# Optimization experiments

Measured on AMD Instinct MI355X. Metric: run time of the kernel, lower is better.

The kernel has to match this reference:

```python
import jax, jax.numpy as jnp
import numpy as np

EPS = 1e-12  # clamp before sqrt, matching torch cdist-style euclidean_dist stability


def euclidean_dist(x, y):
    # x: (N, D), y: (M, D) -> (N, M)
    x2 = jnp.sum(x * x, axis=-1, keepdims=True)          # (N, 1)
    y2 = jnp.sum(y * y, axis=-1)                          # (M,)
    d2 = x2 + y2 - 2.0 * (x @ y.T)
    return jnp.sqrt(jnp.clip(d2, EPS))


def setup_inputs() -> dict:
    key = jax.random.key(0)
    k1, k2 = jax.random.split(key)
    B, W, H, D, M = 8, 28, 28, 128, 16384
    embedding = jax.random.normal(k1, (B * W * H, D), dtype=jnp.float32)
    memory_bank = jax.random.normal(k2, (M, D), dtype=jnp.float32)
    return {"embedding": embedding, "memory_bank": memory_bank,
            "batch_size": B, "width": W, "height": H}


def reference(embedding, memory_bank, batch_size, width, height):
    num_neighbors = 9
    B = batch_size
    D = embedding.shape[-1]
    Mb = memory_bank.shape[0]

    # get_nearest_neighbors with num_neighbors=1 (topk smallest)
    dist = euclidean_dist(embedding, memory_bank)                 # (N, M) -- dominant cost
    neg_vals, locations = jax.lax.top_k(-dist, 1)                 # smallest-1
    patch_scores = (-neg_vals).reshape(B, -1)                     # (B, P)
    locations = locations.reshape(B, -1)                          # (B, P)

    # compute_anomaly_score (num_neighbors > 1 branch)
    b = jnp.arange(B)
    max_patches = jnp.argmax(patch_scores, axis=1)                # (B,)
    emb3 = embedding.reshape(B, -1, D)
    max_patches_features = emb3[b, max_patches]                   # (B, D)
    score = patch_scores[b, max_patches]                          # (B,)
    nn_index = locations[b, max_patches]                          # (B,)
    nn_sample = memory_bank[nn_index]                             # (B, D)

    k = min(num_neighbors, Mb)
    d_nn = euclidean_dist(nn_sample, memory_bank)                 # (B, M)
    _, support_samples = jax.lax.top_k(-d_nn, k)                  # (B, k) smallest-k
    support_feats = memory_bank[support_samples]                  # (B, k, D)

    # batched euclidean dist: (B,1,D) vs (B,k,D) -> (B,k)
    x = max_patches_features[:, None, :]
    d2 = (jnp.sum(x * x, -1) + jnp.sum(support_feats * support_feats, -1)
          - 2.0 * jnp.einsum('bid,bkd->bk', x, support_feats))
    distances = jnp.sqrt(jnp.clip(d2, EPS))                       # (B, k)

    weights = (1.0 - jax.nn.softmax(distances, axis=1))[:, 0]     # (B,)
    return weights * score
```

## Files before the change

### kernel.cpp

```cpp
#include <hip/hip_runtime.h>
#include <cstdint>

#define N_EMB 6272
#define DIMD  128
#define M_BANK 16384
#define BATCH 8
#define PPB   784
#define KNN   9
#define EPSF  1e-12f
#define NKB   64

typedef unsigned long long u64;
typedef _Float16 f16x8 __attribute__((ext_vector_type(8)));
typedef _Float16 f16x2 __attribute__((ext_vector_type(2)));
typedef float    f32x4 __attribute__((ext_vector_type(4)));

static __device__ __forceinline__ u64 umin64(u64 a, u64 b) { return b < a ? b : a; }
static __device__ __forceinline__ u64 umax64(u64 a, u64 b) { return b > a ? b : a; }

static __device__ __forceinline__ void gll16(const _Float16* g, _Float16* l) {
    __builtin_amdgcn_global_load_lds(
        (__attribute__((address_space(1))) void*)(const void*)g,
        (__attribute__((address_space(3))) void*)l, 16, 0, 0);
}

static __device__ __forceinline__ float dot8(f16x8 a, f16x8 b, float c) {
#if __has_builtin(__builtin_amdgcn_fdot2)
    const f16x2* pa = (const f16x2*)&a;
    const f16x2* pb = (const f16x2*)&b;
    c = __builtin_amdgcn_fdot2(pa[0], pb[0], c, false);
    c = __builtin_amdgcn_fdot2(pa[1], pb[1], c, false);
    c = __builtin_amdgcn_fdot2(pa[2], pb[2], c, false);
    c = __builtin_amdgcn_fdot2(pa[3], pb[3], c, false);
#else
    #pragma unroll
    for (int e = 0; e < 8; ++e) c += (float)a[e] * (float)b[e];
#endif
    return c;
}

__global__ __launch_bounds__(256) void convert_kernel(
        const float* __restrict__ emb, const float* __restrict__ bank,
        _Float16* __restrict__ GAh, _Float16* __restrict__ GBh,
        float* __restrict__ x2, float* __restrict__ y2,
        u64* __restrict__ packed) {
    const int gid = blockIdx.x * 256 + threadIdx.x;
    if (gid < N_EMB) packed[gid] = ~0ull;
    const int row = gid >> 4;
    const int chunk = gid & 15;
    const float* src;
    _Float16* dh;
    float* nrm;
    int R;
    if (row < M_BANK) {
        src = bank + (size_t)row * DIMD; dh = GBh; nrm = y2; R = row;
    } else {
        R = row - M_BANK;
        src = emb + (size_t)R * DIMD; dh = GAh; nrm = x2;
    }
    float4 v0 = ((const float4*)src)[chunk * 2];
    float4 v1 = ((const float4*)src)[chunk * 2 + 1];
    float f[8] = {v0.x, v0.y, v0.z, v0.w, v1.x, v1.y, v1.z, v1.w};
    f16x8 h;
    float s = 0.f;
    #pragma unroll
    for (int e = 0; e < 8; ++e) {
        h[e] = (_Float16)f[e];
        s += f[e] * f[e];
    }
    const int q = chunk >> 2, jj = chunk & 3;
    const int jj2 = jj ^ ((R >> 1) & 3);
    *(f16x8*)(dh + (size_t)R * DIMD + q * 32 + jj2 * 8) = h;
    #pragma unroll
    for (int off = 1; off < 16; off <<= 1) s += __shfl_xor(s, off, 16);
    if (chunk == 0) nrm[R] = s;
}


static __device__ __forceinline__ void stageB(
        const _Float16* __restrict__ GBh, _Float16* dst,
        int mrow0, int h, int srow, int se8) {
    #pragma unroll
    for (int j = 0; j < 2; ++j) {
        const int row = srow + j * 64;
        #pragma unroll
        for (int q = 0; q < 2; ++q)
            gll16(GBh + (size_t)(mrow0 + row) * DIMD + h * 64 + q * 32 + se8,
                  dst + q * 4096 + row * 32 + se8);
    }
}

template<int H>
static __device__ __forceinline__ void computeB(
        const _Float16* bb, const f16x8 (&a)[4][4], f32x4 (&acc)[4][4],
        int wm, int g, int r16) {
    f16x8 b[4][2];
    #pragma unroll
    for (int fj = 0; fj < 4; ++fj) {
        const int row = wm * 64 + fj * 16 + r16;
        const int sw = (g ^ ((row >> 1) & 3)) << 3;
        b[fj][0] = *(const f16x8*)&bb[row * 32 + sw];
        b[fj][1] = *(const f16x8*)&bb[4096 + row * 32 + sw];
    }
    #pragma unroll
    for (int ks = 0; ks < 2; ++ks)
        #pragma unroll
        for (int fi = 0; fi < 4; ++fi)
            #pragma unroll
            for (int fj = 0; fj < 4; ++fj)
                acc[fi][fj] = __builtin_amdgcn_mfma_f32_16x16x32_f16(
                    a[fi][2 * H + ks], b[fj][ks], acc[fi][fj], 0, 0, 0);
}

__global__ __launch_bounds__(256, 2) void dist_min_mfma(
        const _Float16* __restrict__ GAh, const _Float16* __restrict__ GBh,
        const float* __restrict__ x2, const float* __restrict__ y2,
        u64* __restrict__ packed) {
    __shared__ _Float16 smem[16384];

    const int bid = blockIdx.x;
    const int c   = bid & 15;
    const int nt  = bid >> 4;
    const int n0  = nt * 128;
    const int mbase = c * 1024;

    const int tid  = threadIdx.x;
    const int lane = tid & 63;
    const int wid  = tid >> 6;
    const int wn = wid >> 1, wm = wid & 1;
    const int g = lane >> 4, r16 = lane & 15;
    const int srow = tid >> 2;
    const int se8  = (tid & 3) * 8;

    _Float16* sB0 = smem;
    _Float16* sB1 = smem + 8192;

    float xs[4][4];
    #pragma unroll
    for (int fi = 0; fi < 4; ++fi)
        #pragma unroll
        for (int r = 0; r < 4; ++r)
            xs[fi][r] = x2[n0 + wn * 64 + fi * 16 + g * 4 + r];

    f16x8 a[4][4];
    #pragma unroll
    for (int h = 0; h < 2; ++h) {
        #pragma unroll
        for (int k = 0; k < 2; ++k)
            #pragma unroll
            for (int j = 0; j < 2; ++j) {
                const int row = srow + j * 64;
                gll16(GAh + (size_t)(n0 + row) * DIMD + (h * 2 + k) * 32 + se8,
                      smem + k * 4096 + row * 32 + se8);
            }
        __syncthreads();
        #pragma unroll
        for (int fi = 0; fi < 4; ++fi) {
            const int row = wn * 64 + fi * 16 + r16;
            const int sw = (g ^ ((row >> 1) & 3)) << 3;
            #pragma unroll
            for (int k = 0; k < 2; ++k)
                a[fi][h * 2 + k] = *(const f16x8*)&smem[k * 4096 + row * 32 + sw];
        }
        __syncthreads();
    }

    stageB(GBh, sB0, mbase, 0, srow, se8);
    __syncthreads();

    f32x4 acc[4][4];
    #pragma unroll
    for (int fi = 0; fi < 4; ++fi)
        #pragma unroll
        for (int fj = 0; fj < 4; ++fj)
            acc[fi][fj] = (f32x4){0.f, 0.f, 0.f, 0.f};

    float runmin[4][4];
    int   runidx[4][4];
    #pragma unroll
    for (int fi = 0; fi < 4; ++fi)
        #pragma unroll
        for (int r = 0; r < 4; ++r) { runmin[fi][r] = 3.4e38f; runidx[fi][r] = 0; }

    for (int t = 0; t < 8; ++t) {
        const int mt = mbase + t * 128;
        stageB(GBh, sB1, mt, 1, srow, se8);
        computeB<0>(sB0, a, acc, wm, g, r16);
        __syncthreads();
        if (t < 7) stageB(GBh, sB0, mt + 128, 0, srow, se8);
        float ys[4];
        #pragma unroll
        for (int fj = 0; fj < 4; ++fj)
            ys[fj] = y2[mt + wm * 64 + fj * 16 + r16];
        computeB<1>(sB1, a, acc, wm, g, r16);

        const int mwave = mt + wm * 64 + r16;
        #pragma unroll
        for (int fi = 0; fi < 4; ++fi) {
            #pragma unroll
            for (int r = 0; r < 4; ++r) {
                float d0 = fmaxf(fmaf(-2.f, acc[fi][0][r], xs[fi][r] + ys[0]), EPSF);
                float d1 = fmaxf(fmaf(-2.f, acc[fi][1][r], xs[fi][r] + ys[1]), EPSF);
                float d2v = fmaxf(fmaf(-2.f, acc[fi][2][r], xs[fi][r] + ys[2]), EPSF);
                float d3 = fmaxf(fmaf(-2.f, acc[fi][3][r], xs[fi][r] + ys[3]), EPSF);
                float m01 = fminf(d0, d1);  int i01 = d1 < d0 ? 1 : 0;
                float m23 = fminf(d2v, d3); int i23 = d3 < d2v ? 3 : 2;
                float tm  = fminf(m01, m23); int ti = m23 < m01 ? i23 : i01;
                if (tm < runmin[fi][r]) {
                    runmin[fi][r] = tm;
                    runidx[fi][r] = mwave + ti * 16;
                }
            }
            #pragma unroll
            for (int fj = 0; fj < 4; ++fj)
                acc[fi][fj] = (f32x4){0.f, 0.f, 0.f, 0.f};
        }
        __syncthreads();
    }

    #pragma unroll
    for (int fi = 0; fi < 4; ++fi) {
        #pragma unroll
        for (int r = 0; r < 4; ++r) {
            const int n = n0 + wn * 64 + fi * 16 + g * 4 + r;
            u64 best = ((u64)__float_as_uint(runmin[fi][r]) << 32)
                     | (unsigned)runidx[fi][r];
            #pragma unroll
            for (int off = 1; off < 16; off <<= 1)
                best = umin64(best, (u64)__shfl_xor((unsigned long long)best, off));
            if (r16 == 0) atomicMin(&packed[n], best);
        }
    }
}

__global__ __launch_bounds__(256) void knn_kernel(
        const u64* __restrict__ packed,
        const _Float16* __restrict__ GBh,
        const float* __restrict__ y2,
        u64* __restrict__ cand) {
    const int b = blockIdx.y, tid = threadIdx.x;
    __shared__ u64 red[256];
    __shared__ u64 red4[4];
    __shared__ u64 s_wkey;
    __shared__ unsigned s_nn;
    __shared__ _Float16 nv[DIMD];

    u64 bk = 0;
    for (int p = tid; p < PPB; p += 256) {
        u64 pk = packed[(size_t)b * PPB + p];
        u64 key = ((pk >> 32) << 32) | (u64)(0xFFFFFFFFu - (unsigned)p);
        bk = umax64(bk, key);
    }
    red[tid] = bk; __syncthreads();
    for (int s = 128; s; s >>= 1) {
        if (tid < s) red[tid] = umax64(red[tid], red[tid + s]);
        __syncthreads();
    }
    if (tid == 0) {
        unsigned p = 0xFFFFFFFFu - (unsigned)red[0];
        s_nn = (unsigned)packed[(size_t)b * PPB + p];
    }
    __syncthreads();
    const unsigned nn = s_nn;
    if (tid < DIMD) nv[tid] = GBh[(size_t)nn * DIMD + tid];
    __syncthreads();

    const int m = blockIdx.x * 256 + tid;
    const int delta = (((nn >> 1) ^ (m >> 1)) & 3);
    const _Float16* row = GBh + (size_t)m * DIMD;
    float dot = 0.f;
    #pragma unroll
    for (int q = 0; q < 4; ++q)
        #pragma unroll
        for (int jj2 = 0; jj2 < 4; ++jj2) {
            f16x8 ym = *(const f16x8*)(row + q * 32 + jj2 * 8);
            f16x8 xm = *(const f16x8*)&nv[q * 32 + (jj2 ^ delta) * 8];
            dot = dot8(ym, xm, dot);
        }
    float d2 = fmaxf(y2[nn] + y2[m] - 2.0f * dot, EPSF);
    const u64 mykey = ((u64)__float_as_uint(d2) << 32) | (unsigned)m;

    u64* myout = cand + ((size_t)b * NKB + blockIdx.x) * KNN;
    bool used = false;
    for (int r = 0; r < KNN; ++r) {
        u64 h = used ? ~0ull : mykey;
        #pragma unroll
        for (int off = 1; off < 64; off <<= 1)
            h = umin64(h, (u64)__shfl_xor((unsigned long long)h, off));
        if ((tid & 63) == 0) red4[tid >> 6] = h;
        __syncthreads();
        if (tid == 0) {
            u64 w = umin64(umin64(red4[0], red4[1]), umin64(red4[2], red4[3]));
            s_wkey = w;
            myout[r] = w;
        }
        __syncthreads();
        if (!used && mykey == s_wkey) used = true;
    }
}

__global__ __launch_bounds__(256) void final_kernel(
        const u64* __restrict__ packed,
        const float* __restrict__ emb, const float* __restrict__ bank,
        const float* __restrict__ x2, const float* __restrict__ y2,
        const u64* __restrict__ cand,
        float* __restrict__ out) {
    const int b = blockIdx.x, tid = threadIdx.x;
    __shared__ u64 lists[256 * 3];
    __shared__ u64 red[256];
    __shared__ float fred[256];
    __shared__ u64 red4[4];
    __shared__ u64 s_wkey;
    __shared__ unsigned s_p, s_nn;
    __shared__ float s_d2star;
    __shared__ unsigned s_sel[KNN];
    __shared__ float s_dist[KNN];
    __shared__ float xv[DIMD];

    u64 bk = 0;
    for (int p = tid; p < PPB; p += 256) {
        u64 pk = packed[(size_t)b * PPB + p];
        u64 key = ((pk >> 32) << 32) | (u64)(0xFFFFFFFFu - (unsigned)p);
        bk = umax64(bk, key);
    }
    red[tid] = bk; __syncthreads();
    for (int s = 128; s; s >>= 1) {
        if (tid < s) red[tid] = umax64(red[tid], red[tid + s]);
        __syncthreads();
    }
    if (tid == 0) {
        unsigned p = 0xFFFFFFFFu - (unsigned)red[0];
        s_p = p;
        s_nn = (unsigned)packed[(size_t)b * PPB + p];
    }
    __syncthreads();
    const unsigned p = s_p, nn = s_nn;

    float prod = 0.f;
    if (tid < DIMD) {
        float xvv = emb[(size_t)(b * PPB + p) * DIMD + tid];
        xv[tid] = xvv;
        prod = xvv * bank[(size_t)nn * DIMD + tid];
    }
    fred[tid] = prod; __syncthreads();
    for (int s = 128; s; s >>= 1) {
        if (tid < s) fred[tid] += fred[tid + s];
        __syncthreads();
    }
    if (tid == 0) {
        float d2 = x2[b * PPB + p] + y2[nn] - 2.0f * fred[0];
        s_d2star = fmaxf(d2, EPSF);
    }

    u64 lst[3] = {~0ull, ~0ull, ~0ull};
    #pragma unroll
    for (int i = 0; i < 3; ++i) {
        const int idx = tid * 3 + i;
        if (idx < NKB * KNN) {
            u64 k = cand[(size_t)b * NKB * KNN + idx];
            lst[2] = k;
            u64 a0 = lst[0], a1 = lst[1], a2 = lst[2];
            u64 t01l = umin64(a0, a1), t01h = umax64(a0, a1);
            u64 m2 = umin64(t01h, a2), h2 = umax64(t01h, a2);
            lst[0] = umin64(t01l, m2);
            lst[1] = umax64(t01l, m2);
            lst[2] = h2;
        }
    }
    lists[tid * 3 + 0] = lst[0];
    lists[tid * 3 + 1] = lst[1];
    lists[tid * 3 + 2] = lst[2];
    __syncthreads();

    int pp = 0;
    for (int r = 0; r < KNN; ++r) {
        u64 h = (pp < 3) ? lists[tid * 3 + pp] : ~0ull;
        #pragma unroll
        for (int off = 1; off < 64; off <<= 1)
            h = umin64(h, (u64)__shfl_xor((unsigned long long)h, off));
        if ((tid & 63) == 0) red4[tid >> 6] = h;
        __syncthreads();
        if (tid == 0) {
            u64 w = umin64(umin64(red4[0], red4[1]), umin64(red4[2], red4[3]));
            s_wkey = w;
            s_sel[r] = (unsigned)w;
        }
        __syncthreads();
        const u64 w = s_wkey;
        if (pp < 3 && lists[tid * 3 + pp] == w) ++pp;
    }

    if (tid < KNN) {
        const unsigned s = s_sel[tid];
        const float* srow = bank + (size_t)s * DIMD;
        float dot = 0.f;
        for (int d = 0; d < DIMD; ++d) dot += srow[d] * xv[d];
        float d2 = x2[b * PPB + p] + y2[s] - 2.0f * dot;
        s_dist[tid] = sqrtf(fmaxf(d2, EPSF));
    }
    __syncthreads();

    if (tid == 0) {
        float mx = s_dist[0];
        for (int i = 1; i < KNN; ++i) mx = fmaxf(mx, s_dist[i]);
        float sum = 0.f, e0 = 0.f;
        for (int i = 0; i < KNN; ++i) {
            float e = expf(s_dist[i] - mx);
            sum += e;
            if (i == 0) e0 = e;
        }
        float w = 1.0f - e0 / sum;
        out[b] = w * sqrtf(s_d2star);
    }
}

extern "C" void kernel_launch(void* const* d_in, const int* in_sizes, int n_in,
                              void* d_out, int out_size, void* d_ws, size_t ws_size,
                              hipStream_t stream) {
    const float* emb  = (const float*)d_in[0];
    const float* bank = (const float*)d_in[1];
    float* out = (float*)d_out;

    char* ws = (char*)d_ws;
    u64*      packed = (u64*)      (ws + 0);
    float*    x2     = (float*)    (ws + 65536);
    float*    y2     = (float*)    (ws + 131072);
    u64*      cand   = (u64*)      (ws + 200704);
    _Float16* GAh    = (_Float16*) (ws + 262144);
    _Float16* GBh    = (_Float16*) (ws + 1867776);

    {
        const int rows = M_BANK + N_EMB;
        const int blocks = rows * 16 / 256;
        convert_kernel<<<blocks, 256, 0, stream>>>(emb, bank, GAh, GBh, x2, y2, packed);
    }

    dist_min_mfma<<<49 * 16, 256, 0, stream>>>(GAh, GBh, x2, y2, packed);

    knn_kernel<<<dim3(NKB, BATCH), 256, 0, stream>>>(packed, GBh, y2, cand);

    final_kernel<<<BATCH, 256, 0, stream>>>(packed, emb, bank, x2, y2, cand, out);
}
```

Measured before the change: 82.04 us.

## Drop argmin tracking from distance kernel; recover nearest neighbor in separate pass

The main MFMA kernel now tracks only the per-row minimum of y2-2xy (adding x2 and the clamp once at the end), with no index bookkeeping, and uses a 32-bit atomicMin in place of a 64-bit packed value. A new nn_find kernel picks the max-score patch per batch and recomputes its exact fp32 distance to every bank entry to recover the nearest-neighbor index and score. Accumulator zeroing is folded into the first MFMA of each tile. The aim is to cut VALU work and register pressure in the hot epilogue, at the cost of an extra kernel launch and one more pass over the bank. Because the argmax patch is chosen from fp16-based scores, the recovered neighbor can in principle differ at near-ties.

```diff
diff --git a/kernel.cpp b/kernel.cpp
--- a/kernel.cpp
+++ b/kernel.cpp
@@ -43,9 +43,10 @@
         const float* __restrict__ emb, const float* __restrict__ bank,
         _Float16* __restrict__ GAh, _Float16* __restrict__ GBh,
         float* __restrict__ x2, float* __restrict__ y2,
-        u64* __restrict__ packed) {
+        unsigned* __restrict__ packed32, u64* __restrict__ binfo) {
     const int gid = blockIdx.x * 256 + threadIdx.x;
-    if (gid < N_EMB) packed[gid] = ~0ull;
+    if (gid < N_EMB) packed32[gid] = 0x7f800000u;
+    if (gid < BATCH) binfo[gid] = ~0ull;
     const int row = gid >> 4;
     const int chunk = gid & 15;
     const float* src;
@@ -90,7 +91,7 @@
     }
 }
 
-template<int H>
+template<int H, bool FIRST>
 static __device__ __forceinline__ void computeB(
         const _Float16* bb, const f16x8 (&a)[4][4], f32x4 (&acc)[4][4],
         int wm, int g, int r16) {
@@ -102,6 +103,7 @@
         b[fj][0] = *(const f16x8*)&bb[row * 32 + sw];
         b[fj][1] = *(const f16x8*)&bb[4096 + row * 32 + sw];
     }
+    const f32x4 zero = {0.f, 0.f, 0.f, 0.f};
     #pragma unroll
     for (int ks = 0; ks < 2; ++ks)
         #pragma unroll
@@ -109,13 +111,14 @@
             #pragma unroll
             for (int fj = 0; fj < 4; ++fj)
                 acc[fi][fj] = __builtin_amdgcn_mfma_f32_16x16x32_f16(
-                    a[fi][2 * H + ks], b[fj][ks], acc[fi][fj], 0, 0, 0);
+                    a[fi][2 * H + ks], b[fj][ks],
+                    (FIRST && ks == 0) ? zero : acc[fi][fj], 0, 0, 0);
 }
 
 __global__ __launch_bounds__(256, 2) void dist_min_mfma(
         const _Float16* __restrict__ GAh, const _Float16* __restrict__ GBh,
         const float* __restrict__ x2, const float* __restrict__ y2,
-        u64* __restrict__ packed) {
+        unsigned* __restrict__ packed32) {
     __shared__ _Float16 smem[16384];
 
     const int bid = blockIdx.x;
@@ -135,13 +138,6 @@
     _Float16* sB0 = smem;
     _Float16* sB1 = smem + 8192;
 
-    float xs[4][4];
-    #pragma unroll
-    for (int fi = 0; fi < 4; ++fi)
-        #pragma unroll
-        for (int r = 0; r < 4; ++r)
-            xs[fi][r] = x2[n0 + wn * 64 + fi * 16 + g * 4 + r];
-
     f16x8 a[4][4];
     #pragma unroll
     for (int h = 0; h < 2; ++h) {
@@ -169,52 +165,35 @@
     __syncthreads();
 
     f32x4 acc[4][4];
+    float runmin[4][4];
     #pragma unroll
     for (int fi = 0; fi < 4; ++fi)
         #pragma unroll
-        for (int fj = 0; fj < 4; ++fj)
-            acc[fi][fj] = (f32x4){0.f, 0.f, 0.f, 0.f};
-
-    float runmin[4][4];
-    int   runidx[4][4];
-    #pragma unroll
-    for (int fi = 0; fi < 4; ++fi)
-        #pragma unroll
-        for (int r = 0; r < 4; ++r) { runmin[fi][r] = 3.4e38f; runidx[fi][r] = 0; }
+        for (int r = 0; r < 4; ++r) runmin[fi][r] = 3.4e38f;
 
     for (int t = 0; t < 8; ++t) {
         const int mt = mbase + t * 128;
         stageB(GBh, sB1, mt, 1, srow, se8);
-        computeB<0>(sB0, a, acc, wm, g, r16);
+        computeB<0, true>(sB0, a, acc, wm, g, r16);
         __syncthreads();
         if (t < 7) stageB(GBh, sB0, mt + 128, 0, srow, se8);
         float ys[4];
         #pragma unroll
         for (int fj = 0; fj < 4; ++fj)
             ys[fj] = y2[mt + wm * 64 + fj * 16 + r16];
-        computeB<1>(sB1, a, acc, wm, g, r16);
-
-        const int mwave = mt + wm * 64 + r16;
-        #pragma unroll
-        for (int fi = 0; fi < 4; ++fi) {
+        computeB<1, false>(sB1, a, acc, wm, g, r16);
+
+        #pragma unroll
+        for (int fi = 0; fi < 4; ++fi)
             #pragma unroll
             for (int r = 0; r < 4; ++r) {
-                float d0 = fmaxf(fmaf(-2.f, acc[fi][0][r], xs[fi][r] + ys[0]), EPSF);
-                float d1 = fmaxf(fmaf(-2.f, acc[fi][1][r], xs[fi][r] + ys[1]), EPSF);
-                float d2v = fmaxf(fmaf(-2.f, acc[fi][2][r], xs[fi][r] + ys[2]), EPSF);
-                float d3 = fmaxf(fmaf(-2.f, acc[fi][3][r], xs[fi][r] + ys[3]), EPSF);
-                float m01 = fminf(d0, d1);  int i01 = d1 < d0 ? 1 : 0;
-                float m23 = fminf(d2v, d3); int i23 = d3 < d2v ? 3 : 2;
-                float tm  = fminf(m01, m23); int ti = m23 < m01 ? i23 : i01;
-                if (tm < runmin[fi][r]) {
-                    runmin[fi][r] = tm;
-                    runidx[fi][r] = mwave + ti * 16;
-                }
+                float d0 = fmaf(-2.f, acc[fi][0][r], ys[0]);
+                float d1 = fmaf(-2.f, acc[fi][1][r], ys[1]);
+                float d2v = fmaf(-2.f, acc[fi][2][r], ys[2]);
+                float d3 = fmaf(-2.f, acc[fi][3][r], ys[3]);
+                runmin[fi][r] = fminf(runmin[fi][r],
+                                      fminf(fminf(d0, d1), fminf(d2v, d3)));
             }
-            #pragma unroll
-            for (int fj = 0; fj < 4; ++fj)
-                acc[fi][fj] = (f32x4){0.f, 0.f, 0.f, 0.f};
-        }
         __syncthreads();
     }
 
@@ -223,45 +202,71 @@
         #pragma unroll
         for (int r = 0; r < 4; ++r) {
             const int n = n0 + wn * 64 + fi * 16 + g * 4 + r;
-            u64 best = ((u64)__float_as_uint(runmin[fi][r]) << 32)
-                     | (unsigned)runidx[fi][r];
+            float v = runmin[fi][r];
             #pragma unroll
             for (int off = 1; off < 16; off <<= 1)
-                best = umin64(best, (u64)__shfl_xor((unsigned long long)best, off));
-            if (r16 == 0) atomicMin(&packed[n], best);
-        }
-    }
+                v = fminf(v, __shfl_xor(v, off));
+            if (r16 == 0) {
+                float d2 = fmaxf(x2[n] + v, EPSF);
+                atomicMin(&packed32[n], __float_as_uint(d2));
+            }
+        }
+    }
+}
+
+__global__ __launch_bounds__(256) void nn_find(
+        const unsigned* __restrict__ packed32,
+        const float* __restrict__ emb, const float* __restrict__ bank,
+        const float* __restrict__ x2, const float* __restrict__ y2,
+        u64* __restrict__ binfo, unsigned* __restrict__ pstar) {
+    const int b = blockIdx.y, tid = threadIdx.x;
+    __shared__ u64 red[256];
+    __shared__ unsigned s_p;
+    __shared__ float xv[DIMD];
+
+    u64 bk = 0;
+    for (int p = tid; p < PPB; p += 256) {
+        unsigned bits = packed32[(size_t)b * PPB + p];
+        u64 key = ((u64)bits << 32) | (u64)(0xFFFFFFFFu - (unsigned)p);
+        bk = umax64(bk, key);
+    }
+    red[tid] = bk; __syncthreads();
+    for (int s = 128; s; s >>= 1) {
+        if (tid < s) red[tid] = umax64(red[tid], red[tid + s]);
+        __syncthreads();
+    }
+    if (tid == 0) s_p = 0xFFFFFFFFu - (unsigned)red[0];
+    __syncthreads();
+    const unsigned p = s_p;
+    if (blockIdx.x == 0 && tid == 0) pstar[b] = p;
+
+    if (tid < DIMD) xv[tid] = emb[(size_t)(b * PPB + p) * DIMD + tid];
+    const float xr2 = x2[b * PPB + p];
+    __syncthreads();
+
+    const int m = blockIdx.x * 256 + tid;
+    const float4* row = (const float4*)(bank + (size_t)m * DIMD);
+    float dot = 0.f;
+    #pragma unroll
+    for (int q = 0; q < DIMD / 4; ++q) {
+        float4 v = row[q];
+        dot += v.x * xv[q*4+0] + v.y * xv[q*4+1] + v.z * xv[q*4+2] + v.w * xv[q*4+3];
+    }
+    float d2 = fmaxf(xr2 + y2[m] - 2.0f * dot, EPSF);
+    atomicMin(&binfo[b], ((u64)__float_as_uint(d2) << 32) | (unsigned)m);
 }
 
 __global__ __launch_bounds__(256) void knn_kernel(
-        const u64* __restrict__ packed,
+        const u64* __restrict__ binfo,
         const _Float16* __restrict__ GBh,
         const float* __restrict__ y2,
         u64* __restrict__ cand) {
     const int b = blockIdx.y, tid = threadIdx.x;
-    __shared__ u64 red[256];
     __shared__ u64 red4[4];
     __shared__ u64 s_wkey;
-    __shared__ unsigned s_nn;
     __shared__ _Float16 nv[DIMD];
 
-    u64 bk = 0;
-    for (int p = tid; p < PPB; p += 256) {
-        u64 pk = packed[(size_t)b * PPB + p];
-        u64 key = ((pk >> 32) << 32) | (u64)(0xFFFFFFFFu - (unsigned)p);
-        bk = umax64(bk, key);
-    }
-    red[tid] = bk; __syncthreads();
-    for (int s = 128; s; s >>= 1) {
-        if (tid < s) red[tid] = umax64(red[tid], red[tid + s]);
-        __syncthreads();
-    }
-    if (tid == 0) {
-        unsigned p = 0xFFFFFFFFu - (unsigned)red[0];
-        s_nn = (unsigned)packed[(size_t)b * PPB + p];
-    }
-    __syncthreads();
-    const unsigned nn = s_nn;
+    const unsigned nn = (unsigned)binfo[b];
     if (tid < DIMD) nv[tid] = GBh[(size_t)nn * DIMD + tid];
     __syncthreads();
 
@@ -300,57 +305,23 @@
 }
 
 __global__ __launch_bounds__(256) void final_kernel(
-        const u64* __restrict__ packed,
         const float* __restrict__ emb, const float* __restrict__ bank,
         const float* __restrict__ x2, const float* __restrict__ y2,
+        const u64* __restrict__ binfo, const unsigned* __restrict__ pstar,
         const u64* __restrict__ cand,
         float* __restrict__ out) {
     const int b = blockIdx.x, tid = threadIdx.x;
     __shared__ u64 lists[256 * 3];
-    __shared__ u64 red[256];
-    __shared__ float fred[256];
     __shared__ u64 red4[4];
     __shared__ u64 s_wkey;
-    __shared__ unsigned s_p, s_nn;
-    __shared__ float s_d2star;
     __shared__ unsigned s_sel[KNN];
     __shared__ float s_dist[KNN];
     __shared__ float xv[DIMD];
 
-    u64 bk = 0;
-    for (int p = tid; p < PPB; p += 256) {
-        u64 pk = packed[(size_t)b * PPB + p];
-        u64 key = ((pk >> 32) << 32) | (u64)(0xFFFFFFFFu - (unsigned)p);
-        bk = umax64(bk, key);
-    }
-    red[tid] = bk; __syncthreads();
-    for (int s = 128; s; s >>= 1) {
-        if (tid < s) red[tid] = umax64(red[tid], red[tid + s]);
-        __syncthreads();
-    }
-    if (tid == 0) {
-        unsigned p = 0xFFFFFFFFu - (unsigned)red[0];
-        s_p = p;
-        s_nn = (unsigned)packed[(size_t)b * PPB + p];
-    }
-    __syncthreads();
-    const unsigned p = s_p, nn = s_nn;
-
-    float prod = 0.f;
-    if (tid < DIMD) {
-        float xvv = emb[(size_t)(b * PPB + p) * DIMD + tid];
-        xv[tid] = xvv;
-        prod = xvv * bank[(size_t)nn * DIMD + tid];
-    }
-    fred[tid] = prod; __syncthreads();
-    for (int s = 128; s; s >>= 1) {
-        if (tid < s) fred[tid] += fred[tid + s];
-        __syncthreads();
-    }
-    if (tid == 0) {
-        float d2 = x2[b * PPB + p] + y2[nn] - 2.0f * fred[0];
-        s_d2star = fmaxf(d2, EPSF);
-    }
+    const unsigned p = pstar[b];
+    const u64 info = binfo[b];
+    const float d2star = __uint_as_float((unsigned)(info >> 32));
+    if (tid < DIMD) xv[tid] = emb[(size_t)(b * PPB + p) * DIMD + tid];
 
     u64 lst[3] = {~0ull, ~0ull, ~0ull};
     #pragma unroll
@@ -410,7 +381,7 @@
             if (i == 0) e0 = e;
         }
         float w = 1.0f - e0 / sum;
-        out[b] = w * sqrtf(s_d2star);
+        out[b] = w * sqrtf(fmaxf(d2star, EPSF));
     }
 }
 
@@ -422,22 +393,29 @@
     float* out = (float*)d_out;
 
     char* ws = (char*)d_ws;
-    u64*      packed = (u64*)      (ws + 0);
-    float*    x2     = (float*)    (ws + 65536);
-    float*    y2     = (float*)    (ws + 131072);
-    u64*      cand   = (u64*)      (ws + 200704);
-    _Float16* GAh    = (_Float16*) (ws + 262144);
-    _Float16* GBh    = (_Float16*) (ws + 1867776);
+    unsigned* packed32 = (unsigned*) (ws + 0);
+    float*    x2       = (float*)    (ws + 32768);
+    float*    y2       = (float*)    (ws + 65536);
+    u64*      binfo    = (u64*)      (ws + 131072);
+    unsigned* pstar    = (unsigned*) (ws + 131200);
+    u64*      cand     = (u64*)      (ws + 135168);
+    _Float16* GAh      = (_Float16*) (ws + 262144);
+    _Float16* GBh      = (_Float16*) (ws + 1867776);
 
     {
         const int rows = M_BANK + N_EMB;
         const int blocks = rows * 16 / 256;
-        convert_kernel<<<blocks, 256, 0, stream>>>(emb, bank, GAh, GBh, x2, y2, packed);
-    }
-
-    dist_min_mfma<<<49 * 16, 256, 0, stream>>>(GAh, GBh, x2, y2, packed);
-
-    knn_kernel<<<dim3(NKB, BATCH), 256, 0, stream>>>(packed, GBh, y2, cand);
-
-    final_kernel<<<BATCH, 256, 0, stream>>>(packed, emb, bank, x2, y2, cand, out);
-}
+        convert_kernel<<<blocks, 256, 0, stream>>>(emb, bank, GAh, GBh, x2, y2,
+                                                   packed32, binfo);
+    }
+
+    dist_min_mfma<<<49 * 16, 256, 0, stream>>>(GAh, GBh, x2, y2, packed32);
+
+    nn_find<<<dim3(NKB, BATCH), 256, 0, stream>>>(packed32, emb, bank, x2, y2,
+                                                  binfo, pstar);
+
+    knn_kernel<<<dim3(NKB, BATCH), 256, 0, stream>>>(binfo, GBh, y2, cand);
+
+    final_kernel<<<BATCH, 256, 0, stream>>>(emb, bank, x2, y2, binfo, pstar,
+                                            cand, out);
+}
```

After: 102.8 us. 1.25x slower.
